# Kernel optimization log

Hardware: AMD Instinct MI355X
Metric: run time of the kernel (lower is better)

Reference implementation:

```python
import jax, jax.numpy as jnp
import numpy as np

N_ATOMS = 500_000
N_DOMAINS = 250_000
N_ENTRIES = 4_000_000
C_IN = 64
C_OUT = 128


def setup_inputs() -> dict:
    key = jax.random.key(0)
    k1, k2, k3, k4 = jax.random.split(key, 4)
    features = jax.random.normal(k1, (N_ATOMS, C_IN), dtype=jnp.float32)
    atom_indices = jax.random.randint(k2, (N_ENTRIES,), 0, N_ATOMS, dtype=jnp.int64)
    domain_ids = jnp.sort(jax.random.randint(k3, (N_ENTRIES,), 0, N_DOMAINS, dtype=jnp.int64))
    # Linear params: xavier_uniform for w, zeros for b (per Linear.reset_parameters)
    limit = jnp.sqrt(6.0 / (C_IN + C_OUT)).astype(jnp.float32)
    W = jax.random.uniform(k4, (C_IN, C_OUT), dtype=jnp.float32, minval=-limit, maxval=limit)
    b = jnp.zeros((C_OUT,), dtype=jnp.float32)
    return {
        "features": features,
        "atom_indices": atom_indices,
        "domain_ids": domain_ids,
        "num_domains": N_DOMAINS,
        "W": W,
        "b": b,
    }


def reference(features, atom_indices, domain_ids, num_domains, W, b):
    # transfer0 (sum reduction): each target domain sums the ptensor0 features
    # of the source atoms it contains. Irregular gather + segment-reduce.
    gathered = features[atom_indices]                       # [E, C_in]
    transferred = jax.ops.segment_sum(gathered, domain_ids,
                                      num_segments=num_domains)  # [M, C_in]
    # Linear projection (mult_factor(0,0)=1 so in_channels unchanged)
    return transferred @ W + b                              # [M, C_out]
```

## Files before the change

### kernel.cpp

```cpp
#include <hip/hip_runtime.h>

__global__ void bounds_kernel(const int* __restrict__ dids,
                              int* __restrict__ starts,
                              int* __restrict__ ends, int E) {
    int e = blockIdx.x * blockDim.x + threadIdx.x;
    if (e >= E) return;
    int d = dids[e];
    if (e == 0) {
        starts[d] = 0;
    } else {
        int dp = dids[e - 1];
        if (d != dp) {
            starts[d] = e;
            ends[dp]  = e;
        }
    }
    if (e == E - 1) ends[d] = E;
}

__global__ void seg_sum_kernel(const float* __restrict__ feat,
                               const int* __restrict__ aidx,
                               const int* __restrict__ starts,
                               const int* __restrict__ ends,
                               float* __restrict__ T, int M) {
    int wid  = (int)(((size_t)blockIdx.x * blockDim.x + threadIdx.x) >> 6);
    if (wid >= M) return;
    int lane = threadIdx.x & 63;

    int s = starts[wid];
    int e = ends[wid];

    float acc = 0.f;
    if (s >= 0) {
        for (int base = s; base < e; base += 16) {
            int rem  = e - base;
            int last = e - 1;
            int ii[16];
#pragma unroll
            for (int j = 0; j < 16; ++j) {
                int t = base + j;
                ii[j] = aidx[t < e ? t : last];
            }
            float v[16];
#pragma unroll
            for (int j = 0; j < 16; ++j)
                v[j] = feat[(size_t)ii[j] * 64 + lane];
#pragma unroll
            for (int j = 0; j < 16; ++j)
                acc += (j < rem) ? v[j] : 0.f;
        }
    }
    T[(size_t)wid * 64 + lane] = acc;
}

#define TM 64
__global__ void __launch_bounds__(256)
proj_kernel(const float* __restrict__ T,
            const float* __restrict__ W,
            const float* __restrict__ bias,
            float* __restrict__ out, int M) {
    __shared__ float lds_w[64][128];
    __shared__ float lds_t[64][TM + 4];

    int tid  = threadIdx.x;
    int row0 = blockIdx.x * TM;

#pragma unroll
    for (int i = 0; i < 8; ++i) {
        int idx = tid + i * 256;
        int k   = idx >> 5;
        int ch  = idx & 31;
        float4 wv = ((const float4*)W)[idx];
        *(float4*)&lds_w[k][ch * 4] = wv;
    }
#pragma unroll
    for (int i = 0; i < 4; ++i) {
        int idx = tid + i * 256;
        int r   = idx >> 4;
        int ch  = idx & 15;
        long gr = row0 + r;
        if (gr > (long)M - 1) gr = M - 1;
        float4 tv = ((const float4*)(T + gr * 64))[ch];
        lds_t[ch * 4 + 0][r] = tv.x;
        lds_t[ch * 4 + 1][r] = tv.y;
        lds_t[ch * 4 + 2][r] = tv.z;
        lds_t[ch * 4 + 3][r] = tv.w;
    }
    __syncthreads();

    int c0 = (tid & 31) * 4;
    int r0 = (tid >> 5) * 8;

    float acc[8][4];
#pragma unroll
    for (int r = 0; r < 8; ++r)
#pragma unroll
        for (int c = 0; c < 4; ++c) acc[r][c] = 0.f;

#pragma unroll 8
    for (int k = 0; k < 64; ++k) {
        float4 ta = *(const float4*)&lds_t[k][r0];
        float4 tb = *(const float4*)&lds_t[k][r0 + 4];
        float4 wv = *(const float4*)&lds_w[k][c0];
        float t[8] = {ta.x, ta.y, ta.z, ta.w, tb.x, tb.y, tb.z, tb.w};
        float w[4] = {wv.x, wv.y, wv.z, wv.w};
#pragma unroll
        for (int r = 0; r < 8; ++r)
#pragma unroll
            for (int c = 0; c < 4; ++c)
                acc[r][c] = fmaf(t[r], w[c], acc[r][c]);
    }

    float4 bv = *(const float4*)&bias[c0];
#pragma unroll
    for (int r = 0; r < 8; ++r) {
        long row = row0 + r0 + r;
        if (row < M) {
            float4 o;
            o.x = acc[r][0] + bv.x;
            o.y = acc[r][1] + bv.y;
            o.z = acc[r][2] + bv.z;
            o.w = acc[r][3] + bv.w;
            *(float4*)&out[row * 128 + c0] = o;
        }
    }
}

extern "C" void kernel_launch(void* const* d_in, const int* in_sizes, int n_in,
                              void* d_out, int out_size, void* d_ws, size_t ws_size,
                              hipStream_t stream) {
    const float* feat = (const float*)d_in[0];
    const int*   aidx = (const int*)d_in[1];
    const int*   dids = (const int*)d_in[2];
    const float* W    = (const float*)d_in[4];
    const float* bias = (const float*)d_in[5];
    float*       out  = (float*)d_out;

    int E = in_sizes[1];
    int M = out_size / 128;

    float* T = (float*)d_ws;
    size_t tbytes = (size_t)M * 64 * sizeof(float);
    size_t bbytes = 2 * (size_t)M * sizeof(int);

    int* starts;
    if (ws_size >= tbytes + bbytes) {
        starts = (int*)((char*)d_ws + tbytes);
    } else {
        starts = (int*)((char*)d_out + (size_t)out_size * sizeof(float) - bbytes);
    }
    int* ends = starts + M;

    hipMemsetAsync(starts, 0xFF, bbytes, stream);

    bounds_kernel<<<(E + 255) / 256, 256, 0, stream>>>(dids, starts, ends, E);

    int waves_blocks = (int)(((size_t)M * 64 + 255) / 256);
    seg_sum_kernel<<<waves_blocks, 256, 0, stream>>>(feat, aidx, starts, ends, T, M);

    proj_kernel<<<(M + TM - 1) / TM, 256, 0, stream>>>(T, W, bias, out, M);
}
```

Before: 424.0 us.

## Gather features with float4 loads across four row groups per wave

```diff
diff --git a/kernel.cpp b/kernel.cpp
--- a/kernel.cpp
+++ b/kernel.cpp
@@ -26,31 +26,54 @@
     int wid  = (int)(((size_t)blockIdx.x * blockDim.x + threadIdx.x) >> 6);
     if (wid >= M) return;
     int lane = threadIdx.x & 63;
+    int g    = lane >> 4;
+    int l16  = lane & 15;
+    int coff = l16 * 4;
 
     int s = starts[wid];
     int e = ends[wid];
 
-    float acc = 0.f;
+    float4 acc = make_float4(0.f, 0.f, 0.f, 0.f);
     if (s >= 0) {
+        int last = e - 1;
         for (int base = s; base < e; base += 16) {
-            int rem  = e - base;
-            int last = e - 1;
-            int ii[16];
+            int rem = e - base;
+            int ti  = base + l16;
+            int idxv = aidx[ti <= last ? ti : last];
+            if (rem >= 16) {
 #pragma unroll
-            for (int j = 0; j < 16; ++j) {
-                int t = base + j;
-                ii[j] = aidx[t < e ? t : last];
+                for (int p = 0; p < 4; ++p) {
+                    int row = __shfl(idxv, p * 4 + g, 64);
+                    const float4 v =
+                        *(const float4*)(feat + (size_t)row * 64 + coff);
+                    acc.x += v.x; acc.y += v.y; acc.z += v.z; acc.w += v.w;
+                }
+            } else {
+                int nph = (rem + 3) >> 2;
+                for (int p = 0; p < nph; ++p) {
+                    int t   = base + p * 4 + g;
+                    int row = __shfl(idxv, p * 4 + g, 64);
+                    const float4 v =
+                        *(const float4*)(feat + (size_t)row * 64 + coff);
+                    float w = (t <= last) ? 1.f : 0.f;
+                    acc.x = fmaf(v.x, w, acc.x);
+                    acc.y = fmaf(v.y, w, acc.y);
+                    acc.z = fmaf(v.z, w, acc.z);
+                    acc.w = fmaf(v.w, w, acc.w);
+                }
             }
-            float v[16];
-#pragma unroll
-            for (int j = 0; j < 16; ++j)
-                v[j] = feat[(size_t)ii[j] * 64 + lane];
-#pragma unroll
-            for (int j = 0; j < 16; ++j)
-                acc += (j < rem) ? v[j] : 0.f;
         }
+        acc.x += __shfl_xor(acc.x, 16, 64);
+        acc.y += __shfl_xor(acc.y, 16, 64);
+        acc.z += __shfl_xor(acc.z, 16, 64);
+        acc.w += __shfl_xor(acc.w, 16, 64);
+        acc.x += __shfl_xor(acc.x, 32, 64);
+        acc.y += __shfl_xor(acc.y, 32, 64);
+        acc.z += __shfl_xor(acc.z, 32, 64);
+        acc.w += __shfl_xor(acc.w, 32, 64);
     }
-    T[(size_t)wid * 64 + lane] = acc;
+    if (g == 0)
+        *(float4*)(T + (size_t)wid * 64 + coff) = acc;
 }
 
 #define TM 64
```

New measurement: 417.2 us. Within noise of the previous version (-1.6%).
